# Optimization experiments

Hardware: AMD Instinct MI355X
Metric: run time of the kernel (lower is better)

Reference implementation:

```python
import jax, jax.numpy as jnp
import numpy as np

W_CD = 1.0   # cfg TRAIN.LOSS_WEIGHT_CHAMFER_DISTANCE
W_RV = 1.0   # cfg TRAIN.LOSS_WEIGHT_RANGE_VIEW
W_MASK = 1.0 # cfg TRAIN.LOSS_WEIGHT_MASK


def setup_inputs() -> dict:
    key = jax.random.key(0)
    k0, k1, k2, k3, k4 = jax.random.split(key, 5)
    B, T, H, W = 2, 5, 64, 2048   # batch, future steps, range-image dims
    N = M = 4096                  # n_samples (TEST.N_DOWNSAMPLED_POINTS_CD)
    output_rv = jax.random.normal(k0, (B, T, H, W), jnp.float32)
    mask_logits = jax.random.normal(k1, (B, T, H, W), jnp.float32)
    target_range_image = jax.random.normal(k2, (B, T, H, W), jnp.float32)
    output_points = jax.random.normal(k3, (B, T, N, 3), jnp.float32)
    target_points = jax.random.normal(k4, (B, T, M, 3), jnp.float32)
    return {
        "output_rv": output_rv,
        "mask_logits": mask_logits,
        "output_points": output_points,
        "target_points": target_points,
        "target_range_image": target_range_image,
    }


def _chamfer(output_points, target_points):
    on = jnp.sum(output_points * output_points, axis=-1)            # [B,T,N]
    tn = jnp.sum(target_points * target_points, axis=-1)            # [B,T,M]
    cross = jnp.einsum('btnd,btmd->btnm', output_points, target_points)
    d2 = on[..., :, None] + tn[..., None, :] - 2.0 * cross          # [B,T,N,M]
    dist1 = jnp.min(d2, axis=-1).mean(axis=-1)                      # [B,T] out->tgt NN
    dist2 = jnp.min(d2, axis=-2).mean(axis=-1)                      # [B,T] tgt->out NN
    cd_bt = dist1 + dist2                                           # per (b,s) CD
    return cd_bt.T, jnp.mean(cd_bt)                                 # [T,B] tensor, scalar mean


def reference(output_rv, mask_logits, output_points, target_points, target_range_image):
    # L1 range loss: output values are forced to -1 wherever target == -1
    out_m = jnp.where(target_range_image == -1.0, -1.0, output_rv)
    loss_rv = jnp.mean(jnp.abs(out_m - target_range_image))
    # mask BCE-with-logits: target mask is 1 where range view is valid (> 0)
    tmask = (target_range_image > 0.0).astype(output_rv.dtype)
    x = mask_logits
    loss_mask = jnp.mean(jnp.maximum(x, 0.0) - x * tmask + jnp.log1p(jnp.exp(-jnp.abs(x))))
    # Chamfer distance over fixed-size subsampled point clouds
    cd_tensor, loss_cd = _chamfer(output_points, target_points)
    total = W_CD * loss_cd + W_RV * loss_rv + W_MASK * loss_mask
    return total, cd_tensor, loss_cd, loss_rv, loss_mask
```

## Files before the change

kernel.cpp:

```cpp
#include <hip/hip_runtime.h>
#include <math.h>

#define BB 2
#define TT 5
#define NPTS 4096
#define NBT (BB * TT)
#define NELEM (BB * TT * 64 * 2048)

#define EW_BLOCKS 640
#define CH_BLOCKS 1280
#define QPB 64
#define NQC 64

#define EW1 1280
#define EW2 1920

typedef _Float16 h8 __attribute__((ext_vector_type(8)));
typedef float f32x16 __attribute__((ext_vector_type(16)));
typedef float f32x4 __attribute__((ext_vector_type(4)));

__device__ inline unsigned pkh(float a, float b) {
    union { _Float16 h[2]; unsigned u; } c;
    c.h[0] = (_Float16)a;
    c.h[1] = (_Float16)b;
    return c.u;
}

__global__ __launch_bounds__(256) void main_kernel(
        const float4* __restrict__ rv4,
        const float4* __restrict__ lg4,
        const float4* __restrict__ tg4,
        const float* __restrict__ OP,
        const float* __restrict__ TP,
        float* __restrict__ ws) {
    __shared__ __align__(16) uint2 pts[4096];
    __shared__ float nqlds[QPB];
    __shared__ float qmin[2][QPB];
    int bid = blockIdx.x;
    int tid = threadIdx.x;
    int lane = tid & 63;
    int wave = tid >> 6;

    if (bid < EW_BLOCKS) {
        float srv = 0.0f, smk = 0.0f;
        int base = (bid * 256 + tid) * 2;
#pragma unroll
        for (int u = 0; u < 2; ++u) {
            int i = base + u;
            float4 o4 = rv4[i];
            float4 x4 = lg4[i];
            float4 t4 = tg4[i];
            const float* op = &o4.x;
            const float* xp = &x4.x;
            const float* tp = &t4.x;
#pragma unroll
            for (int j = 0; j < 4; ++j) {
                float tv = tp[j];
                float ov = (tv == -1.0f) ? -1.0f : op[j];
                srv += fabsf(ov - tv);
                float tm = (tv > 0.0f) ? 1.0f : 0.0f;
                float xv = xp[j];
                smk += fmaxf(xv, 0.0f) - xv * tm + __logf(1.0f + __expf(-fabsf(xv)));
            }
        }
#pragma unroll
        for (int off = 32; off > 0; off >>= 1) {
            srv += __shfl_down(srv, off);
            smk += __shfl_down(smk, off);
        }
        __shared__ float s1[4], s2[4];
        if (lane == 0) { s1[wave] = srv; s2[wave] = smk; }
        __syncthreads();
        if (tid == 0) {
            ws[EW1 + bid] = s1[0] + s1[1] + s1[2] + s1[3];
            ws[EW2 + bid] = s2[0] + s2[1] + s2[2] + s2[3];
        }
        return;
    }

    int cb = bid - EW_BLOCKS;
    int dir = cb / (NBT * NQC);
    int rem = cb % (NBT * NQC);
    int bt = rem / NQC;
    int qc = rem % NQC;
    const float* P = dir ? TP : OP;
    const float* Q = dir ? OP : TP;
    const float* Pb = P + (size_t)bt * NPTS * 3;
    const float* Qb = Q + (size_t)bt * NPTS * 3;

    int qrow = lane & 31;
    int wq = wave & 1;
    int ph = wave >> 1;

    int qidx = qc * QPB + wq * 32 + qrow;
    float qx = 0.0f, qy = 0.0f, qz = 0.0f;
    if (lane < 32) {
        const float* p = Pb + (size_t)qidx * 3;
        qx = p[0]; qy = p[1]; qz = p[2];
        nqlds[wq * 32 + qrow] = fmaf(qx, qx, fmaf(qy, qy, qz * qz));
    }
    union { unsigned u[4]; h8 h; } ua;
    ua.u[0] = ua.u[1] = ua.u[2] = ua.u[3] = 0u;
    if (lane < 32) {
        ua.u[0] = pkh(-2.0f * qx, -2.0f * qy);
        ua.u[1] = pkh(-2.0f * qz, 1.0f);
    }
    h8 afrag = ua.h;

#pragma unroll
    for (int t = 0; t < 4; ++t) {
        int pt0 = t * 1024 + tid * 4;
        const f32x4* src = (const f32x4*)(Qb + (size_t)pt0 * 3);
        f32x4 c0 = src[0], c1 = src[1], c2 = src[2];
        float x0 = c0[0], y0 = c0[1], z0 = c0[2];
        float x1 = c0[3], y1 = c1[0], z1 = c1[1];
        float x2 = c1[2], y2 = c1[3], z2 = c2[0];
        float x3 = c2[1], y3 = c2[2], z3 = c2[3];
        float n0 = fmaf(x0, x0, fmaf(y0, y0, z0 * z0));
        float n1 = fmaf(x1, x1, fmaf(y1, y1, z1 * z1));
        float n2 = fmaf(x2, x2, fmaf(y2, y2, z2 * z2));
        float n3 = fmaf(x3, x3, fmaf(y3, y3, z3 * z3));
        uint4* dst = (uint4*)&pts[t * 1024 + tid * 4];
        dst[0] = make_uint4(pkh(x0, y0), pkh(z0, n0), pkh(x1, y1), pkh(z1, n1));
        dst[1] = make_uint4(pkh(x2, y2), pkh(z2, n2), pkh(x3, y3), pkh(z3, n3));
    }
    __syncthreads();

    const f32x16 zc = {0.0f, 0.0f, 0.0f, 0.0f, 0.0f, 0.0f, 0.0f, 0.0f,
                       0.0f, 0.0f, 0.0f, 0.0f, 0.0f, 0.0f, 0.0f, 0.0f};
    float vm[16];
#pragma unroll
    for (int r = 0; r < 16; ++r) vm[r] = INFINITY;

    union { unsigned u[4]; h8 h; } ub0, ub1, ub2, ub3;
    ub0.u[2] = ub0.u[3] = 0u;
    ub1.u[2] = ub1.u[3] = 0u;
    ub2.u[2] = ub2.u[3] = 0u;
    ub3.u[2] = ub3.u[3] = 0u;

    const uint2* pb = pts + ph * 2048 + qrow;
#pragma unroll
    for (int g = 0; g < 16; ++g) {
        uint2 b0 = pb[g * 128 + 0 * 32];
        uint2 b1 = pb[g * 128 + 1 * 32];
        uint2 b2 = pb[g * 128 + 2 * 32];
        uint2 b3 = pb[g * 128 + 3 * 32];
        ub0.u[0] = b0.x; ub0.u[1] = b0.y;
        ub1.u[0] = b1.x; ub1.u[1] = b1.y;
        ub2.u[0] = b2.x; ub2.u[1] = b2.y;
        ub3.u[0] = b3.x; ub3.u[1] = b3.y;
        f32x16 d0 = __builtin_amdgcn_mfma_f32_32x32x16_f16(afrag, ub0.h, zc, 0, 0, 0);
        f32x16 d1 = __builtin_amdgcn_mfma_f32_32x32x16_f16(afrag, ub1.h, zc, 0, 0, 0);
        f32x16 d2 = __builtin_amdgcn_mfma_f32_32x32x16_f16(afrag, ub2.h, zc, 0, 0, 0);
        f32x16 d3 = __builtin_amdgcn_mfma_f32_32x32x16_f16(afrag, ub3.h, zc, 0, 0, 0);
#pragma unroll
        for (int r = 0; r < 16; ++r) {
            float a = d0[r], c = d1[r];
            asm("v_min3_f32 %0, %0, %1, %2" : "+v"(vm[r]) : "v"(a), "v"(c));
        }
#pragma unroll
        for (int r = 0; r < 16; ++r) {
            float a = d2[r], c = d3[r];
            asm("v_min3_f32 %0, %0, %1, %2" : "+v"(vm[r]) : "v"(a), "v"(c));
        }
    }

#pragma unroll
    for (int r = 0; r < 16; ++r) {
        float m = vm[r];
        m = fminf(m, __shfl_xor(m, 1));
        m = fminf(m, __shfl_xor(m, 2));
        m = fminf(m, __shfl_xor(m, 4));
        m = fminf(m, __shfl_xor(m, 8));
        m = fminf(m, __shfl_xor(m, 16));
        vm[r] = m;
    }
    if ((lane & 31) == 0) {
        int half = lane >> 5;
#pragma unroll
        for (int r = 0; r < 16; ++r) {
            int row = (r & 3) + 8 * (r >> 2) + 4 * half;
            qmin[ph][wq * 32 + row] = vm[r];
        }
    }
    __syncthreads();

    if (wave == 0) {
        float m = fminf(qmin[0][lane], qmin[1][lane]) + nqlds[lane];
#pragma unroll
        for (int off = 32; off > 0; off >>= 1) m += __shfl_down(m, off);
        if (lane == 0) ws[cb] = m;
    }
}

__global__ void finalize_kernel(const float* __restrict__ ws, float* __restrict__ out) {
    __shared__ float grp[20];
    __shared__ float ra[4], rb[4];
    int tid = threadIdx.x;
    int lane = tid & 63;
    int wave = tid >> 6;

    for (int g = wave; g < 20; g += 4) {
        float s = ws[g * 64 + lane];
#pragma unroll
        for (int off = 32; off > 0; off >>= 1) s += __shfl_down(s, off);
        if (lane == 0) grp[g] = s;
    }

    float sa = 0.0f, sb = 0.0f;
    for (int i = tid; i < EW_BLOCKS; i += 256) {
        sa += ws[EW1 + i];
        sb += ws[EW2 + i];
    }
#pragma unroll
    for (int off = 32; off > 0; off >>= 1) {
        sa += __shfl_down(sa, off);
        sb += __shfl_down(sb, off);
    }
    if (lane == 0) { ra[wave] = sa; rb[wave] = sb; }
    __syncthreads();

    if (tid == 0) {
        const float inv_e = 1.0f / (float)NELEM;
        float loss_rv = (ra[0] + ra[1] + ra[2] + ra[3]) * inv_e;
        float loss_mask = (rb[0] + rb[1] + rb[2] + rb[3]) * inv_e;
        float cd_sum = 0.0f;
        for (int bt = 0; bt < NBT; ++bt) {
            float cd = (grp[bt] + grp[NBT + bt]) * (1.0f / NPTS);
            int b = bt / TT;
            int t = bt % TT;
            out[1 + t * BB + b] = cd;
            cd_sum += cd;
        }
        float loss_cd = cd_sum / (float)NBT;
        out[0] = loss_cd + loss_rv + loss_mask;
        out[11] = loss_cd;
        out[12] = loss_rv;
        out[13] = loss_mask;
    }
}

extern "C" void kernel_launch(void* const* d_in, const int* in_sizes, int n_in,
                              void* d_out, int out_size, void* d_ws, size_t ws_size,
                              hipStream_t stream) {
    const float* output_rv = (const float*)d_in[0];
    const float* mask_logits = (const float*)d_in[1];
    const float* output_points = (const float*)d_in[2];
    const float* target_points = (const float*)d_in[3];
    const float* target_rv = (const float*)d_in[4];
    float* out = (float*)d_out;
    float* ws = (float*)d_ws;

    main_kernel<<<EW_BLOCKS + CH_BLOCKS, 256, 0, stream>>>(
        (const float4*)output_rv, (const float4*)mask_logits,
        (const float4*)target_rv, output_points, target_points, ws);

    finalize_kernel<<<1, 256, 0, stream>>>(ws, out);
}
```

Before: 30.39 us.

## Pre-pack point clouds to fp16 in a prep kernel, read packed data from global

A prep kernel now converts each point cloud once into packed fp16 (x,y,z,|p|^2) records in the workspace, and it also runs the elementwise loss blocks. A separate chamfer kernel reads these packed records straight from global memory (L2-resident) instead of having every block reload and repack 4096 fp32 points into LDS. This removes redundant per-block conversion, LDS staging and a block barrier. In exchange it adds an extra kernel launch with a serial dependency, relies on cached global loads inside the MFMA loop, and reduces unrolling of that loop to 4.

```diff
diff --git a/kernel.cpp b/kernel.cpp
--- a/kernel.cpp
+++ b/kernel.cpp
@@ -7,6 +7,7 @@
 #define NBT (BB * TT)
 #define NELEM (BB * TT * 64 * 2048)
 
+#define PACK_BLOCKS 40
 #define EW_BLOCKS 640
 #define CH_BLOCKS 1280
 #define QPB 64
@@ -14,6 +15,7 @@
 
 #define EW1 1280
 #define EW2 1920
+#define PKF 2560
 
 typedef _Float16 h8 __attribute__((ext_vector_type(8)));
 typedef float f32x16 __attribute__((ext_vector_type(16)));
@@ -26,14 +28,86 @@
     return c.u;
 }
 
-__global__ __launch_bounds__(256) void main_kernel(
+__global__ __launch_bounds__(256) void prep_kernel(
         const float4* __restrict__ rv4,
         const float4* __restrict__ lg4,
         const float4* __restrict__ tg4,
         const float* __restrict__ OP,
         const float* __restrict__ TP,
         float* __restrict__ ws) {
-    __shared__ __align__(16) uint2 pts[4096];
+    int bid = blockIdx.x;
+    int tid = threadIdx.x;
+    int lane = tid & 63;
+    int wave = tid >> 6;
+
+    if (bid < PACK_BLOCKS) {
+        int c = bid >> 1;
+        int h = bid & 1;
+        const float* src = (c < NBT) ? (TP + (size_t)c * NPTS * 3)
+                                     : (OP + (size_t)(c - NBT) * NPTS * 3);
+        int pt0 = h * 2048 + tid * 8;
+        const f32x4* s4 = (const f32x4*)(src + (size_t)pt0 * 3);
+        f32x4 v0 = s4[0], v1 = s4[1], v2 = s4[2], v3 = s4[3], v4 = s4[4], v5 = s4[5];
+        float X[8], Y[8], Z[8];
+        X[0]=v0[0]; Y[0]=v0[1]; Z[0]=v0[2];
+        X[1]=v0[3]; Y[1]=v1[0]; Z[1]=v1[1];
+        X[2]=v1[2]; Y[2]=v1[3]; Z[2]=v2[0];
+        X[3]=v2[1]; Y[3]=v2[2]; Z[3]=v2[3];
+        X[4]=v3[0]; Y[4]=v3[1]; Z[4]=v3[2];
+        X[5]=v3[3]; Y[5]=v4[0]; Z[5]=v4[1];
+        X[6]=v4[2]; Y[6]=v4[3]; Z[6]=v5[0];
+        X[7]=v5[1]; Y[7]=v5[2]; Z[7]=v5[3];
+        uint4* d4 = (uint4*)((uint2*)(ws + PKF) + (size_t)c * NPTS + pt0);
+#pragma unroll
+        for (int j = 0; j < 4; ++j) {
+            float n0 = fmaf(X[2*j], X[2*j], fmaf(Y[2*j], Y[2*j], Z[2*j]*Z[2*j]));
+            float n1 = fmaf(X[2*j+1], X[2*j+1], fmaf(Y[2*j+1], Y[2*j+1], Z[2*j+1]*Z[2*j+1]));
+            d4[j] = make_uint4(pkh(X[2*j], Y[2*j]), pkh(Z[2*j], n0),
+                               pkh(X[2*j+1], Y[2*j+1]), pkh(Z[2*j+1], n1));
+        }
+        return;
+    }
+
+    int eb = bid - PACK_BLOCKS;
+    float srv = 0.0f, smk = 0.0f;
+    int base = (eb * 256 + tid) * 2;
+#pragma unroll
+    for (int u = 0; u < 2; ++u) {
+        int i = base + u;
+        float4 o4 = rv4[i];
+        float4 x4 = lg4[i];
+        float4 t4 = tg4[i];
+        const float* op = &o4.x;
+        const float* xp = &x4.x;
+        const float* tp = &t4.x;
+#pragma unroll
+        for (int j = 0; j < 4; ++j) {
+            float tv = tp[j];
+            float ov = (tv == -1.0f) ? -1.0f : op[j];
+            srv += fabsf(ov - tv);
+            float tm = (tv > 0.0f) ? 1.0f : 0.0f;
+            float xv = xp[j];
+            smk += fmaxf(xv, 0.0f) - xv * tm + __logf(1.0f + __expf(-fabsf(xv)));
+        }
+    }
+#pragma unroll
+    for (int off = 32; off > 0; off >>= 1) {
+        srv += __shfl_down(srv, off);
+        smk += __shfl_down(smk, off);
+    }
+    __shared__ float s1[4], s2[4];
+    if (lane == 0) { s1[wave] = srv; s2[wave] = smk; }
+    __syncthreads();
+    if (tid == 0) {
+        ws[EW1 + eb] = s1[0] + s1[1] + s1[2] + s1[3];
+        ws[EW2 + eb] = s2[0] + s2[1] + s2[2] + s2[3];
+    }
+}
+
+__global__ __launch_bounds__(256) void chamfer_kernel(
+        const float* __restrict__ OP,
+        const float* __restrict__ TP,
+        float* __restrict__ ws) {
     __shared__ float nqlds[QPB];
     __shared__ float qmin[2][QPB];
     int bid = blockIdx.x;
@@ -41,52 +115,13 @@
     int lane = tid & 63;
     int wave = tid >> 6;
 
-    if (bid < EW_BLOCKS) {
-        float srv = 0.0f, smk = 0.0f;
-        int base = (bid * 256 + tid) * 2;
-#pragma unroll
-        for (int u = 0; u < 2; ++u) {
-            int i = base + u;
-            float4 o4 = rv4[i];
-            float4 x4 = lg4[i];
-            float4 t4 = tg4[i];
-            const float* op = &o4.x;
-            const float* xp = &x4.x;
-            const float* tp = &t4.x;
-#pragma unroll
-            for (int j = 0; j < 4; ++j) {
-                float tv = tp[j];
-                float ov = (tv == -1.0f) ? -1.0f : op[j];
-                srv += fabsf(ov - tv);
-                float tm = (tv > 0.0f) ? 1.0f : 0.0f;
-                float xv = xp[j];
-                smk += fmaxf(xv, 0.0f) - xv * tm + __logf(1.0f + __expf(-fabsf(xv)));
-            }
-        }
-#pragma unroll
-        for (int off = 32; off > 0; off >>= 1) {
-            srv += __shfl_down(srv, off);
-            smk += __shfl_down(smk, off);
-        }
-        __shared__ float s1[4], s2[4];
-        if (lane == 0) { s1[wave] = srv; s2[wave] = smk; }
-        __syncthreads();
-        if (tid == 0) {
-            ws[EW1 + bid] = s1[0] + s1[1] + s1[2] + s1[3];
-            ws[EW2 + bid] = s2[0] + s2[1] + s2[2] + s2[3];
-        }
-        return;
-    }
-
-    int cb = bid - EW_BLOCKS;
-    int dir = cb / (NBT * NQC);
-    int rem = cb % (NBT * NQC);
+    int dir = bid / (NBT * NQC);
+    int rem = bid % (NBT * NQC);
     int bt = rem / NQC;
     int qc = rem % NQC;
     const float* P = dir ? TP : OP;
-    const float* Q = dir ? OP : TP;
+    const uint2* pk = (const uint2*)(ws + PKF) + (size_t)(dir * NBT + bt) * NPTS;
     const float* Pb = P + (size_t)bt * NPTS * 3;
-    const float* Qb = Q + (size_t)bt * NPTS * 3;
 
     int qrow = lane & 31;
     int wq = wave & 1;
@@ -107,25 +142,6 @@
     }
     h8 afrag = ua.h;
 
-#pragma unroll
-    for (int t = 0; t < 4; ++t) {
-        int pt0 = t * 1024 + tid * 4;
-        const f32x4* src = (const f32x4*)(Qb + (size_t)pt0 * 3);
-        f32x4 c0 = src[0], c1 = src[1], c2 = src[2];
-        float x0 = c0[0], y0 = c0[1], z0 = c0[2];
-        float x1 = c0[3], y1 = c1[0], z1 = c1[1];
-        float x2 = c1[2], y2 = c1[3], z2 = c2[0];
-        float x3 = c2[1], y3 = c2[2], z3 = c2[3];
-        float n0 = fmaf(x0, x0, fmaf(y0, y0, z0 * z0));
-        float n1 = fmaf(x1, x1, fmaf(y1, y1, z1 * z1));
-        float n2 = fmaf(x2, x2, fmaf(y2, y2, z2 * z2));
-        float n3 = fmaf(x3, x3, fmaf(y3, y3, z3 * z3));
-        uint4* dst = (uint4*)&pts[t * 1024 + tid * 4];
-        dst[0] = make_uint4(pkh(x0, y0), pkh(z0, n0), pkh(x1, y1), pkh(z1, n1));
-        dst[1] = make_uint4(pkh(x2, y2), pkh(z2, n2), pkh(x3, y3), pkh(z3, n3));
-    }
-    __syncthreads();
-
     const f32x16 zc = {0.0f, 0.0f, 0.0f, 0.0f, 0.0f, 0.0f, 0.0f, 0.0f,
                        0.0f, 0.0f, 0.0f, 0.0f, 0.0f, 0.0f, 0.0f, 0.0f};
     float vm[16];
@@ -138,8 +154,8 @@
     ub2.u[2] = ub2.u[3] = 0u;
     ub3.u[2] = ub3.u[3] = 0u;
 
-    const uint2* pb = pts + ph * 2048 + qrow;
-#pragma unroll
+    const uint2* pb = pk + ph * 2048 + qrow;
+#pragma unroll 4
     for (int g = 0; g < 16; ++g) {
         uint2 b0 = pb[g * 128 + 0 * 32];
         uint2 b1 = pb[g * 128 + 1 * 32];
@@ -189,7 +205,7 @@
         float m = fminf(qmin[0][lane], qmin[1][lane]) + nqlds[lane];
 #pragma unroll
         for (int off = 32; off > 0; off >>= 1) m += __shfl_down(m, off);
-        if (lane == 0) ws[cb] = m;
+        if (lane == 0) ws[bid] = m;
     }
 }
 
@@ -251,9 +267,11 @@
     float* out = (float*)d_out;
     float* ws = (float*)d_ws;
 
-    main_kernel<<<EW_BLOCKS + CH_BLOCKS, 256, 0, stream>>>(
+    prep_kernel<<<PACK_BLOCKS + EW_BLOCKS, 256, 0, stream>>>(
         (const float4*)output_rv, (const float4*)mask_logits,
         (const float4*)target_rv, output_points, target_points, ws);
 
+    chamfer_kernel<<<CH_BLOCKS, 256, 0, stream>>>(output_points, target_points, ws);
+
     finalize_kernel<<<1, 256, 0, stream>>>(ws, out);
 }
```

New measurement: 32.78 us. 7.9% more time.
